# Performance work log

Hardware: AMD Instinct MI355X
Metric: run time of the kernel (lower is better)

Reference implementation:

```python
import jax, jax.numpy as jnp
import numpy as np

EPS = 1e-12  # torch F.normalize clamp_min eps
NUM_HEADS = 4


def setup_inputs() -> dict:
    key = jax.random.key(0)
    ks = jax.random.split(key, 6)
    B, N, C = 8, 8192, 256
    x1 = jax.random.normal(ks[0], (B, N, C), dtype=jnp.float32)
    x2 = jax.random.normal(ks[1], (B, N, C), dtype=jnp.float32)
    s = 1.0 / np.sqrt(C)
    Wq = jax.random.normal(ks[2], (C, C), dtype=jnp.float32) * s
    Wk = jax.random.normal(ks[3], (C, C), dtype=jnp.float32) * s
    Wv = jax.random.normal(ks[4], (C, C), dtype=jnp.float32) * s
    Wo = jax.random.normal(ks[5], (C, C), dtype=jnp.float32) * s
    bo = jnp.zeros((C,), dtype=jnp.float32)
    temperature = jnp.ones((NUM_HEADS, 1, 1), dtype=jnp.float32)
    return {"x1": x1, "x2": x2, "Wq": Wq, "Wk": Wk, "Wv": Wv,
            "Wo": Wo, "bo": bo, "temperature": temperature}


def reference(x1, x2, Wq, Wk, Wv, Wo, bo, temperature):
    B, N, C = x1.shape
    H = NUM_HEADS
    d = C // H
    # Linear projections (torch Linear: y = x W^T), then [B,H,d,N] layout
    q = (x1 @ Wq.T).reshape(B, N, H, d).transpose(0, 2, 3, 1)  # [B,H,d,N]
    k = (x2 @ Wk.T).reshape(B, N, H, d).transpose(0, 2, 3, 1)  # [B,H,d,N]
    v = (x2 @ Wv.T).reshape(B, N, H, d).transpose(0, 2, 3, 1)  # [B,H,d,N]
    # L2-normalize along the token axis (dim=-1)
    qn = q / jnp.maximum(jnp.linalg.norm(q, axis=-1, keepdims=True), EPS)
    kn = k / jnp.maximum(jnp.linalg.norm(k, axis=-1, keepdims=True), EPS)
    # Channel-wise cross-covariance attention: [B,H,d,d]
    attn = jnp.einsum('bhdn,bhen->bhde', qn, kn) * temperature
    attn = jax.nn.softmax(attn, axis=-1)
    # (dropout is identity in eval mode)
    x_cross = jnp.einsum('bhde,bhen->bhdn', attn, v)  # [B,H,d,N]
    x_cross = x_cross.transpose(0, 3, 1, 2).reshape(B, N, C)  # [B,N,C]
    return x_cross @ Wo.T + bo
```

## Files before the change

### kernel.cpp

```cpp
#include <hip/hip_runtime.h>
#include <hip/hip_bf16.h>

#define BDIM 8
#define NTOK 8192
#define CDIM 256
#define HEADS 4
#define DHEAD 64
#define MROWS (BDIM * NTOK)

typedef unsigned short ushort_t;
typedef short bf16x8 __attribute__((ext_vector_type(8)));
typedef float f32x4 __attribute__((ext_vector_type(4)));
typedef unsigned short u16x8 __attribute__((ext_vector_type(8)));
typedef unsigned short u16x4 __attribute__((ext_vector_type(4)));

__device__ inline ushort_t f2bf(float f) {
    __hip_bfloat16 h = __float2bfloat16(f);
    return *reinterpret_cast<ushort_t*>(&h);
}

__device__ inline u16x8 pack8(float4 a, float4 b) {
    u16x8 o;
    o[0] = f2bf(a.x); o[1] = f2bf(a.y); o[2] = f2bf(a.z); o[3] = f2bf(a.w);
    o[4] = f2bf(b.x); o[5] = f2bf(b.y); o[6] = f2bf(b.z); o[7] = f2bf(b.w);
    return o;
}

__global__ __launch_bounds__(256) void zero_kernel(float* __restrict__ p, int n) {
    int i = blockIdx.x * 256 + threadIdx.x;
    if (i < n) p[i] = 0.0f;
}

__global__ __launch_bounds__(256) void proj_mfma(
    const float* __restrict__ x1, const float* __restrict__ x2,
    const float* __restrict__ Wq, const float* __restrict__ Wk,
    const float* __restrict__ Wv,
    ushort_t* __restrict__ qp, ushort_t* __restrict__ kp, ushort_t* __restrict__ vp,
    float* __restrict__ ssq, float* __restrict__ ssk)
{
    const float* A; const float* W; ushort_t* outp; float* ss;
    if (blockIdx.z == 0)      { A = x1; W = Wq; outp = qp; ss = ssq; }
    else if (blockIdx.z == 1) { A = x2; W = Wk; outp = kp; ss = ssk; }
    else                      { A = x2; W = Wv; outp = vp; ss = nullptr; }

    __shared__ ushort_t Asl[2][4096];
    __shared__ ushort_t Bsl[2][4096];
    __shared__ float colss[128];

    const int t = threadIdx.x;
    const int lane = t & 63, w = t >> 6;
    const int l16 = lane & 15, quad = lane >> 4;
    const int m0 = blockIdx.x * 128, c0 = blockIdx.y * 128;
    const int wm = (w >> 1) * 64, wn = (w & 1) * 64;

    const int srow = t >> 1;
    const int skh  = t & 1;

    const float* Ap = A + (size_t)(m0 + srow) * CDIM + skh * 16;
    const float* Wp = W + (size_t)(c0 + srow) * CDIM + skh * 16;

    float4 ga[4], gb[4];
#pragma unroll
    for (int i = 0; i < 4; ++i) {
        ga[i] = *(const float4*)(Ap + i * 4);
        gb[i] = *(const float4*)(Wp + i * 4);
    }

    f32x4 acc[4][4] = {};

#pragma unroll 2
    for (int it = 0; it < 8; ++it) {
        ushort_t* As = Asl[it & 1];
        ushort_t* Bs = Bsl[it & 1];
        *(u16x8*)&As[(skh * 2 + 0) * 1024 + srow * 8] = pack8(ga[0], ga[1]);
        *(u16x8*)&As[(skh * 2 + 1) * 1024 + srow * 8] = pack8(ga[2], ga[3]);
        *(u16x8*)&Bs[(skh * 2 + 0) * 1024 + srow * 8] = pack8(gb[0], gb[1]);
        *(u16x8*)&Bs[(skh * 2 + 1) * 1024 + srow * 8] = pack8(gb[2], gb[3]);
        if (it < 7) {
            int ko = (it + 1) * 32;
#pragma unroll
            for (int i = 0; i < 4; ++i) {
                ga[i] = *(const float4*)(Ap + ko + i * 4);
                gb[i] = *(const float4*)(Wp + ko + i * 4);
            }
        }
        asm volatile("s_waitcnt lgkmcnt(0)" ::: "memory");
        __builtin_amdgcn_s_barrier();
        bf16x8 aF[4], bF[4];
#pragma unroll
        for (int i = 0; i < 4; ++i)
            aF[i] = *(const bf16x8*)&As[quad * 1024 + (wm + i * 16 + l16) * 8];
#pragma unroll
        for (int j = 0; j < 4; ++j)
            bF[j] = *(const bf16x8*)&Bs[quad * 1024 + (wn + j * 16 + l16) * 8];
#pragma unroll
        for (int i = 0; i < 4; ++i)
#pragma unroll
            for (int j = 0; j < 4; ++j)
                acc[i][j] = __builtin_amdgcn_mfma_f32_16x16x32_bf16(aF[i], bF[j], acc[i][j], 0, 0, 0);
    }

#pragma unroll
    for (int i = 0; i < 4; ++i) {
#pragma unroll
        for (int j = 0; j < 4; ++j) {
            int col = c0 + wn + j * 16 + l16;
#pragma unroll
            for (int reg = 0; reg < 4; ++reg) {
                int row = m0 + wm + i * 16 + quad * 4 + reg;
                outp[(size_t)row * CDIM + col] = f2bf(acc[i][j][reg]);
            }
        }
    }

    if (ss) {
        __syncthreads();
        if (t < 128) colss[t] = 0.0f;
        __syncthreads();
#pragma unroll
        for (int j = 0; j < 4; ++j) {
            float s = 0.0f;
#pragma unroll
            for (int i = 0; i < 4; ++i)
#pragma unroll
                for (int reg = 0; reg < 4; ++reg)
                    s += acc[i][j][reg] * acc[i][j][reg];
            atomicAdd(&colss[wn + j * 16 + l16], s);
        }
        __syncthreads();
        if (t < 128) {
            int b = m0 >> 13;
            atomicAdd(&ss[b * CDIM + c0 + t], colss[t]);
        }
    }
}

__global__ __launch_bounds__(256) void gram_mfma(
    const ushort_t* __restrict__ qp, const ushort_t* __restrict__ kp,
    float* __restrict__ G)
{
    constexpr int NS = 144;
    __shared__ ushort_t qs[64 * NS];
    __shared__ ushort_t ks2[64 * NS];
    __shared__ float gsum[4096];

    const int t = threadIdx.x;
    const int lane = t & 63, w = t >> 6;
    const int l16 = lane & 15, quad = lane >> 4;
    const int slab = blockIdx.x, h = blockIdx.y, b = blockIdx.z;
    const size_t base = (size_t)b * NTOK * CDIM + h * DHEAD;

    const int cg  = t >> 5;
    const int ng4 = t & 31;

    for (int i = t; i < 4096; i += 256) gsum[i] = 0.0f;

    f32x4 acc[4][4] = {};

    for (int n0 = slab * 512; n0 < slab * 512 + 512; n0 += 128) {
        u16x8 qv[4], kv[4];
#pragma unroll
        for (int i = 0; i < 4; ++i) {
            size_t g = base + (size_t)(n0 + ng4 * 4 + i) * CDIM + cg * 8;
            qv[i] = *(const u16x8*)&qp[g];
            kv[i] = *(const u16x8*)&kp[g];
        }
        __syncthreads();
#pragma unroll
        for (int j = 0; j < 8; ++j) {
            u16x4 wq, wk;
            wq[0] = qv[0][j]; wq[1] = qv[1][j]; wq[2] = qv[2][j]; wq[3] = qv[3][j];
            wk[0] = kv[0][j]; wk[1] = kv[1][j]; wk[2] = kv[2][j]; wk[3] = kv[3][j];
            *(u16x4*)&qs[(cg * 8 + j) * NS + ng4 * 4] = wq;
            *(u16x4*)&ks2[(cg * 8 + j) * NS + ng4 * 4] = wk;
        }
        __syncthreads();
        bf16x8 aF[4], bF[4];
#pragma unroll
        for (int i = 0; i < 4; ++i)
            aF[i] = *(const bf16x8*)&qs[(i * 16 + l16) * NS + w * 32 + quad * 8];
#pragma unroll
        for (int j = 0; j < 4; ++j)
            bF[j] = *(const bf16x8*)&ks2[(j * 16 + l16) * NS + w * 32 + quad * 8];
#pragma unroll
        for (int i = 0; i < 4; ++i)
#pragma unroll
            for (int j = 0; j < 4; ++j)
                acc[i][j] = __builtin_amdgcn_mfma_f32_16x16x32_bf16(aF[i], bF[j], acc[i][j], 0, 0, 0);
    }

    __syncthreads();
#pragma unroll
    for (int i = 0; i < 4; ++i)
#pragma unroll
        for (int j = 0; j < 4; ++j)
#pragma unroll
            for (int reg = 0; reg < 4; ++reg)
                atomicAdd(&gsum[(i * 16 + quad * 4 + reg) * 64 + j * 16 + l16], acc[i][j][reg]);
    __syncthreads();

    float* Gp = G + (size_t)(b * HEADS + h) * 4096;
    for (int i = t; i < 4096; i += 256) atomicAdd(&Gp[i], gsum[i]);
}

__global__ __launch_bounds__(64) void attn_softmax(
    float* __restrict__ G, const float* __restrict__ ssq,
    const float* __restrict__ ssk, const float* __restrict__ temp)
{
    const int h = blockIdx.x, b = blockIdx.y;
    const int d = threadIdx.x;
    __shared__ float nk[64];

    float nq = fmaxf(sqrtf(ssq[b * CDIM + h * DHEAD + d]), 1e-12f);
    nk[d]    = fmaxf(sqrtf(ssk[b * CDIM + h * DHEAD + d]), 1e-12f);
    __syncthreads();

    float* row = G + (size_t)(b * HEADS + h) * DHEAD * DHEAD + d * DHEAD;
    const float tmp = temp[h];

    float vals[64];
    float mx = -1e30f;
#pragma unroll
    for (int e = 0; e < 64; ++e) {
        float v = row[e] / (nq * nk[e]) * tmp;
        vals[e] = v;
        mx = fmaxf(mx, v);
    }
    float s = 0.0f;
#pragma unroll
    for (int e = 0; e < 64; ++e) {
        float ev = __expf(vals[e] - mx);
        vals[e] = ev;
        s += ev;
    }
    float inv = 1.0f / s;
#pragma unroll
    for (int e = 0; e < 64; ++e) row[e] = vals[e] * inv;
}

__global__ __launch_bounds__(256) void weff_kernel(
    const float* __restrict__ Wo, const float* __restrict__ attn,
    ushort_t* __restrict__ Weffb)
{
    const int h = blockIdx.x, b = blockIdx.y;
    const int c = threadIdx.x;
    __shared__ float at[64][65];

    const float* Ab = attn + (size_t)(b * HEADS + h) * DHEAD * DHEAD;
    for (int idx = c; idx < DHEAD * DHEAD; idx += 256)
        at[idx >> 6][idx & 63] = Ab[idx];
    __syncthreads();

    float wo[64];
#pragma unroll
    for (int d2 = 0; d2 < 64; ++d2) wo[d2] = Wo[(size_t)c * CDIM + h * DHEAD + d2];

    ushort_t* Wb = Weffb + (size_t)b * CDIM * CDIM + (size_t)c * CDIM + h * DHEAD;
#pragma unroll 4
    for (int e = 0; e < 64; ++e) {
        float s = 0.0f;
#pragma unroll
        for (int d2 = 0; d2 < 64; ++d2) s += wo[d2] * at[d2][e];
        Wb[e] = f2bf(s);
    }
}

__global__ __launch_bounds__(256) void out_mfma(
    const ushort_t* __restrict__ vp, const ushort_t* __restrict__ Weffb,
    const float* __restrict__ bo, float* __restrict__ out)
{
    __shared__ ushort_t Asl[2][4096];
    __shared__ ushort_t Bsl[2][4096];

    const int t = threadIdx.x;
    const int lane = t & 63, w = t >> 6;
    const int l16 = lane & 15, quad = lane >> 4;
    const int m0 = blockIdx.x * 128, c0 = blockIdx.y * 128;
    const int wm = (w >> 1) * 64, wn = (w & 1) * 64;

    const int srow = t >> 1;
    const int skh  = t & 1;

    const ushort_t* Ap = vp + (size_t)(m0 + srow) * CDIM + skh * 16;
    const ushort_t* Bp = Weffb + (size_t)(m0 >> 13) * CDIM * CDIM
                       + (size_t)(c0 + srow) * CDIM + skh * 16;

    u16x8 ga0 = *(const u16x8*)Ap,       ga1 = *(const u16x8*)(Ap + 8);
    u16x8 gb0 = *(const u16x8*)Bp,       gb1 = *(const u16x8*)(Bp + 8);

    f32x4 acc[4][4] = {};

#pragma unroll 2
    for (int it = 0; it < 8; ++it) {
        ushort_t* As = Asl[it & 1];
        ushort_t* Bs = Bsl[it & 1];
        *(u16x8*)&As[(skh * 2 + 0) * 1024 + srow * 8] = ga0;
        *(u16x8*)&As[(skh * 2 + 1) * 1024 + srow * 8] = ga1;
        *(u16x8*)&Bs[(skh * 2 + 0) * 1024 + srow * 8] = gb0;
        *(u16x8*)&Bs[(skh * 2 + 1) * 1024 + srow * 8] = gb1;
        if (it < 7) {
            int ko = (it + 1) * 32;
            ga0 = *(const u16x8*)(Ap + ko);
            ga1 = *(const u16x8*)(Ap + ko + 8);
            gb0 = *(const u16x8*)(Bp + ko);
            gb1 = *(const u16x8*)(Bp + ko + 8);
        }
        asm volatile("s_waitcnt lgkmcnt(0)" ::: "memory");
        __builtin_amdgcn_s_barrier();
        bf16x8 aF[4], bF[4];
#pragma unroll
        for (int i = 0; i < 4; ++i)
            aF[i] = *(const bf16x8*)&As[quad * 1024 + (wm + i * 16 + l16) * 8];
#pragma unroll
        for (int j = 0; j < 4; ++j)
            bF[j] = *(const bf16x8*)&Bs[quad * 1024 + (wn + j * 16 + l16) * 8];
#pragma unroll
        for (int i = 0; i < 4; ++i)
#pragma unroll
            for (int j = 0; j < 4; ++j)
                acc[i][j] = __builtin_amdgcn_mfma_f32_16x16x32_bf16(aF[i], bF[j], acc[i][j], 0, 0, 0);
    }

#pragma unroll
    for (int i = 0; i < 4; ++i) {
#pragma unroll
        for (int j = 0; j < 4; ++j) {
            int col = c0 + wn + j * 16 + l16;
            float bias = bo[col];
#pragma unroll
            for (int reg = 0; reg < 4; ++reg) {
                int row = m0 + wm + i * 16 + quad * 4 + reg;
                out[(size_t)row * CDIM + col] = acc[i][j][reg] + bias;
            }
        }
    }
}

extern "C" void kernel_launch(void* const* d_in, const int* in_sizes, int n_in,
                              void* d_out, int out_size, void* d_ws, size_t ws_size,
                              hipStream_t stream) {
    const float* x1   = (const float*)d_in[0];
    const float* x2   = (const float*)d_in[1];
    const float* Wq   = (const float*)d_in[2];
    const float* Wk   = (const float*)d_in[3];
    const float* Wv   = (const float*)d_in[4];
    const float* Wo   = (const float*)d_in[5];
    const float* bo   = (const float*)d_in[6];
    const float* temp = (const float*)d_in[7];
    float* out = (float*)d_out;

    char* ws = (char*)d_ws;
    const size_t SZP = (size_t)MROWS * CDIM * sizeof(ushort_t);
    ushort_t* qp   = (ushort_t*)(ws);
    ushort_t* kp   = (ushort_t*)(ws + SZP);
    ushort_t* vp   = (ushort_t*)(ws + 2 * SZP);
    float*    ssq  = (float*)(ws + 3 * SZP);
    float*    ssk  = (float*)(ws + 3 * SZP + 8192);
    float*    G    = (float*)(ws + 3 * SZP + 16384);
    ushort_t* Weffb= (ushort_t*)(ws + 3 * SZP + 540672);

    zero_kernel<<<dim3((135168 + 255) / 256), dim3(256), 0, stream>>>(ssq, 135168);

    proj_mfma<<<dim3(MROWS / 128, CDIM / 128, 3), dim3(256), 0, stream>>>(
        x1, x2, Wq, Wk, Wv, qp, kp, vp, ssq, ssk);

    gram_mfma<<<dim3(16, HEADS, BDIM), dim3(256), 0, stream>>>(qp, kp, G);

    attn_softmax<<<dim3(HEADS, BDIM), dim3(64), 0, stream>>>(G, ssq, ssk, temp);

    weff_kernel<<<dim3(HEADS, BDIM), dim3(256), 0, stream>>>(Wo, G, Weffb);

    out_mfma<<<dim3(MROWS / 128, CDIM / 128), dim3(256), 0, stream>>>(vp, Weffb, bo, out);
}
```

Measured before the change: 350.6 us.

## Deepen global prefetch in GEMMs, pipeline gram loads, fuse softmax into Weff kernel

The projection and output GEMMs now prefetch two K-steps ahead using double register buffers, are fully unrolled, and get a min-blocks-per-CU launch bound of 4. The gram kernel double-buffers its q/k global loads so the next chunk's load overlaps the current chunk's LDS transpose and MFMAs. The softmax and Weff kernels are merged into one launch, with the softmax spread across four threads per row using shuffle reductions. This hides more global-load latency and removes one launch plus a G round trip through memory, at the cost of more registers, which could cause spills under the tighter launch bound.

Measured after the change: 487.5 us. 39.0% more time.

```diff
diff --git a/kernel.cpp b/kernel.cpp
--- a/kernel.cpp
+++ b/kernel.cpp
@@ -31,7 +31,7 @@
     if (i < n) p[i] = 0.0f;
 }
 
-__global__ __launch_bounds__(256) void proj_mfma(
+__global__ __launch_bounds__(256, 4) void proj_mfma(
     const float* __restrict__ x1, const float* __restrict__ x2,
     const float* __restrict__ Wq, const float* __restrict__ Wk,
     const float* __restrict__ Wv,
@@ -59,29 +59,32 @@
     const float* Ap = A + (size_t)(m0 + srow) * CDIM + skh * 16;
     const float* Wp = W + (size_t)(c0 + srow) * CDIM + skh * 16;
 
-    float4 ga[4], gb[4];
-#pragma unroll
-    for (int i = 0; i < 4; ++i) {
-        ga[i] = *(const float4*)(Ap + i * 4);
-        gb[i] = *(const float4*)(Wp + i * 4);
-    }
+    float4 ga[2][4], gb[2][4];
+#pragma unroll
+    for (int s = 0; s < 2; ++s)
+#pragma unroll
+        for (int i = 0; i < 4; ++i) {
+            ga[s][i] = *(const float4*)(Ap + s * 32 + i * 4);
+            gb[s][i] = *(const float4*)(Wp + s * 32 + i * 4);
+        }
 
     f32x4 acc[4][4] = {};
 
-#pragma unroll 2
+#pragma unroll
     for (int it = 0; it < 8; ++it) {
-        ushort_t* As = Asl[it & 1];
-        ushort_t* Bs = Bsl[it & 1];
-        *(u16x8*)&As[(skh * 2 + 0) * 1024 + srow * 8] = pack8(ga[0], ga[1]);
-        *(u16x8*)&As[(skh * 2 + 1) * 1024 + srow * 8] = pack8(ga[2], ga[3]);
-        *(u16x8*)&Bs[(skh * 2 + 0) * 1024 + srow * 8] = pack8(gb[0], gb[1]);
-        *(u16x8*)&Bs[(skh * 2 + 1) * 1024 + srow * 8] = pack8(gb[2], gb[3]);
-        if (it < 7) {
-            int ko = (it + 1) * 32;
+        const int p = it & 1;
+        ushort_t* As = Asl[p];
+        ushort_t* Bs = Bsl[p];
+        *(u16x8*)&As[(skh * 2 + 0) * 1024 + srow * 8] = pack8(ga[p][0], ga[p][1]);
+        *(u16x8*)&As[(skh * 2 + 1) * 1024 + srow * 8] = pack8(ga[p][2], ga[p][3]);
+        *(u16x8*)&Bs[(skh * 2 + 0) * 1024 + srow * 8] = pack8(gb[p][0], gb[p][1]);
+        *(u16x8*)&Bs[(skh * 2 + 1) * 1024 + srow * 8] = pack8(gb[p][2], gb[p][3]);
+        if (it < 6) {
+            const int ko = (it + 2) * 32;
 #pragma unroll
             for (int i = 0; i < 4; ++i) {
-                ga[i] = *(const float4*)(Ap + ko + i * 4);
-                gb[i] = *(const float4*)(Wp + ko + i * 4);
+                ga[p][i] = *(const float4*)(Ap + ko + i * 4);
+                gb[p][i] = *(const float4*)(Wp + ko + i * 4);
             }
         }
         asm volatile("s_waitcnt lgkmcnt(0)" ::: "memory");
@@ -157,22 +160,33 @@
 
     f32x4 acc[4][4] = {};
 
-    for (int n0 = slab * 512; n0 < slab * 512 + 512; n0 += 128) {
-        u16x8 qv[4], kv[4];
-#pragma unroll
-        for (int i = 0; i < 4; ++i) {
-            size_t g = base + (size_t)(n0 + ng4 * 4 + i) * CDIM + cg * 8;
-            qv[i] = *(const u16x8*)&qp[g];
-            kv[i] = *(const u16x8*)&kp[g];
-        }
+    u16x8 qv[2][4], kv[2][4];
+#pragma unroll
+    for (int i = 0; i < 4; ++i) {
+        size_t g = base + (size_t)(slab * 512 + ng4 * 4 + i) * CDIM + cg * 8;
+        qv[0][i] = *(const u16x8*)&qp[g];
+        kv[0][i] = *(const u16x8*)&kp[g];
+    }
+
+#pragma unroll
+    for (int cch = 0; cch < 4; ++cch) {
+        const int p = cch & 1;
         __syncthreads();
 #pragma unroll
         for (int j = 0; j < 8; ++j) {
             u16x4 wq, wk;
-            wq[0] = qv[0][j]; wq[1] = qv[1][j]; wq[2] = qv[2][j]; wq[3] = qv[3][j];
-            wk[0] = kv[0][j]; wk[1] = kv[1][j]; wk[2] = kv[2][j]; wk[3] = kv[3][j];
+            wq[0] = qv[p][0][j]; wq[1] = qv[p][1][j]; wq[2] = qv[p][2][j]; wq[3] = qv[p][3][j];
+            wk[0] = kv[p][0][j]; wk[1] = kv[p][1][j]; wk[2] = kv[p][2][j]; wk[3] = kv[p][3][j];
             *(u16x4*)&qs[(cg * 8 + j) * NS + ng4 * 4] = wq;
             *(u16x4*)&ks2[(cg * 8 + j) * NS + ng4 * 4] = wk;
+        }
+        if (cch < 3) {
+#pragma unroll
+            for (int i = 0; i < 4; ++i) {
+                size_t g = base + (size_t)(slab * 512 + (cch + 1) * 128 + ng4 * 4 + i) * CDIM + cg * 8;
+                qv[p ^ 1][i] = *(const u16x8*)&qp[g];
+                kv[p ^ 1][i] = *(const u16x8*)&kp[g];
+            }
         }
         __syncthreads();
         bf16x8 aF[4], bF[4];
@@ -203,54 +217,53 @@
     for (int i = t; i < 4096; i += 256) atomicAdd(&Gp[i], gsum[i]);
 }
 
-__global__ __launch_bounds__(64) void attn_softmax(
-    float* __restrict__ G, const float* __restrict__ ssq,
-    const float* __restrict__ ssk, const float* __restrict__ temp)
+__global__ __launch_bounds__(256) void softmax_weff(
+    const float* __restrict__ G, const float* __restrict__ ssq,
+    const float* __restrict__ ssk, const float* __restrict__ temp,
+    const float* __restrict__ Wo, ushort_t* __restrict__ Weffb)
 {
     const int h = blockIdx.x, b = blockIdx.y;
-    const int d = threadIdx.x;
+    const int t = threadIdx.x;
+    __shared__ float at[64][65];
     __shared__ float nk[64];
 
-    float nq = fmaxf(sqrtf(ssq[b * CDIM + h * DHEAD + d]), 1e-12f);
-    nk[d]    = fmaxf(sqrtf(ssk[b * CDIM + h * DHEAD + d]), 1e-12f);
+    if (t < 64) nk[t] = fmaxf(sqrtf(ssk[b * CDIM + h * DHEAD + t]), 1e-12f);
     __syncthreads();
 
-    float* row = G + (size_t)(b * HEADS + h) * DHEAD * DHEAD + d * DHEAD;
-    const float tmp = temp[h];
-
-    float vals[64];
-    float mx = -1e30f;
-#pragma unroll
-    for (int e = 0; e < 64; ++e) {
-        float v = row[e] / (nq * nk[e]) * tmp;
-        vals[e] = v;
-        mx = fmaxf(mx, v);
-    }
-    float s = 0.0f;
-#pragma unroll
-    for (int e = 0; e < 64; ++e) {
-        float ev = __expf(vals[e] - mx);
-        vals[e] = ev;
-        s += ev;
-    }
-    float inv = 1.0f / s;
-#pragma unroll
-    for (int e = 0; e < 64; ++e) row[e] = vals[e] * inv;
-}
-
-__global__ __launch_bounds__(256) void weff_kernel(
-    const float* __restrict__ Wo, const float* __restrict__ attn,
-    ushort_t* __restrict__ Weffb)
-{
-    const int h = blockIdx.x, b = blockIdx.y;
-    const int c = threadIdx.x;
-    __shared__ float at[64][65];
-
-    const float* Ab = attn + (size_t)(b * HEADS + h) * DHEAD * DHEAD;
-    for (int idx = c; idx < DHEAD * DHEAD; idx += 256)
-        at[idx >> 6][idx & 63] = Ab[idx];
+    {
+        const int row = t >> 2, part = t & 3;
+        const float* Grow = G + (size_t)(b * HEADS + h) * 4096 + row * 64;
+        const float tmp = temp[h];
+        const float nq = fmaxf(sqrtf(ssq[b * CDIM + h * DHEAD + row]), 1e-12f);
+
+        float vals[16];
+        float mx = -1e30f;
+#pragma unroll
+        for (int j = 0; j < 16; ++j) {
+            int e = part * 16 + j;
+            float v = Grow[e] / (nq * nk[e]) * tmp;
+            vals[j] = v;
+            mx = fmaxf(mx, v);
+        }
+        mx = fmaxf(mx, __shfl_xor(mx, 1));
+        mx = fmaxf(mx, __shfl_xor(mx, 2));
+        float s = 0.0f;
+#pragma unroll
+        for (int j = 0; j < 16; ++j) {
+            float ev = __expf(vals[j] - mx);
+            vals[j] = ev;
+            s += ev;
+        }
+        s += __shfl_xor(s, 1);
+        s += __shfl_xor(s, 2);
+        float inv = 1.0f / s;
+#pragma unroll
+        for (int j = 0; j < 16; ++j)
+            at[row][part * 16 + j] = vals[j] * inv;
+    }
     __syncthreads();
 
+    const int c = t;
     float wo[64];
 #pragma unroll
     for (int d2 = 0; d2 < 64; ++d2) wo[d2] = Wo[(size_t)c * CDIM + h * DHEAD + d2];
@@ -265,7 +278,7 @@
     }
 }
 
-__global__ __launch_bounds__(256) void out_mfma(
+__global__ __launch_bounds__(256, 4) void out_mfma(
     const ushort_t* __restrict__ vp, const ushort_t* __restrict__ Weffb,
     const float* __restrict__ bo, float* __restrict__ out)
 {
@@ -285,25 +298,32 @@
     const ushort_t* Bp = Weffb + (size_t)(m0 >> 13) * CDIM * CDIM
                        + (size_t)(c0 + srow) * CDIM + skh * 16;
 
-    u16x8 ga0 = *(const u16x8*)Ap,       ga1 = *(const u16x8*)(Ap + 8);
-    u16x8 gb0 = *(const u16x8*)Bp,       gb1 = *(const u16x8*)(Bp + 8);
+    u16x8 ga[2][2], gb[2][2];
+#pragma unroll
+    for (int s = 0; s < 2; ++s) {
+        ga[s][0] = *(const u16x8*)(Ap + s * 32);
+        ga[s][1] = *(const u16x8*)(Ap + s * 32 + 8);
+        gb[s][0] = *(const u16x8*)(Bp + s * 32);
+        gb[s][1] = *(const u16x8*)(Bp + s * 32 + 8);
+    }
 
     f32x4 acc[4][4] = {};
 
-#pragma unroll 2
+#pragma unroll
     for (int it = 0; it < 8; ++it) {
-        ushort_t* As = Asl[it & 1];
-        ushort_t* Bs = Bsl[it & 1];
-        *(u16x8*)&As[(skh * 2 + 0) * 1024 + srow * 8] = ga0;
-        *(u16x8*)&As[(skh * 2 + 1) * 1024 + srow * 8] = ga1;
-        *(u16x8*)&Bs[(skh * 2 + 0) * 1024 + srow * 8] = gb0;
-        *(u16x8*)&Bs[(skh * 2 + 1) * 1024 + srow * 8] = gb1;
-        if (it < 7) {
-            int ko = (it + 1) * 32;
-            ga0 = *(const u16x8*)(Ap + ko);
-            ga1 = *(const u16x8*)(Ap + ko + 8);
-            gb0 = *(const u16x8*)(Bp + ko);
-            gb1 = *(const u16x8*)(Bp + ko + 8);
+        const int p = it & 1;
+        ushort_t* As = Asl[p];
+        ushort_t* Bs = Bsl[p];
+        *(u16x8*)&As[(skh * 2 + 0) * 1024 + srow * 8] = ga[p][0];
+        *(u16x8*)&As[(skh * 2 + 1) * 1024 + srow * 8] = ga[p][1];
+        *(u16x8*)&Bs[(skh * 2 + 0) * 1024 + srow * 8] = gb[p][0];
+        *(u16x8*)&Bs[(skh * 2 + 1) * 1024 + srow * 8] = gb[p][1];
+        if (it < 6) {
+            const int ko = (it + 2) * 32;
+            ga[p][0] = *(const u16x8*)(Ap + ko);
+            ga[p][1] = *(const u16x8*)(Ap + ko + 8);
+            gb[p][0] = *(const u16x8*)(Bp + ko);
+            gb[p][1] = *(const u16x8*)(Bp + ko + 8);
         }
         asm volatile("s_waitcnt lgkmcnt(0)" ::: "memory");
         __builtin_amdgcn_s_barrier();
@@ -366,9 +386,7 @@
 
     gram_mfma<<<dim3(16, HEADS, BDIM), dim3(256), 0, stream>>>(qp, kp, G);
 
-    attn_softmax<<<dim3(HEADS, BDIM), dim3(64), 0, stream>>>(G, ssq, ssk, temp);
-
-    weff_kernel<<<dim3(HEADS, BDIM), dim3(256), 0, stream>>>(Wo, G, Weffb);
+    softmax_weff<<<dim3(HEADS, BDIM), dim3(256), 0, stream>>>(G, ssq, ssk, temp, Wo, Weffb);
 
     out_mfma<<<dim3(MROWS / 128, CDIM / 128), dim3(256), 0, stream>>>(vp, Weffb, bo, out);
 }
```
